# Kernel optimization log

Measured on AMD Instinct MI355X. Metric: run time of the kernel, lower is better.

Reference implementation:

```python
import jax, jax.numpy as jnp
import numpy as np

D_MODEL = 256
N_LAYERS = 4
D_STATE = 16
D_CONV = 4
EXPAND = 2
HEADDIM = 64
D_INNER = EXPAND * D_MODEL            # 512
NHEADS = D_INNER // HEADDIM           # 8
CONV_DIM = D_INNER + 2 * D_STATE      # 544 (ngroups=1)
D_IN_PROJ = 2 * D_INNER + 2 * D_STATE + NHEADS  # 1064
VOCAB = 8
MAXLEN = 2048
NCLASSES = 2
PAD_IDX = 4
EPS = 1e-5
B, L = 8, 2048


def setup_inputs() -> dict:
    key = jax.random.key(0)
    ks = jax.random.split(key, 10)
    x = jax.random.randint(ks[0], (B, L), 0, VOCAB)
    attention_mask = jnp.ones((B, L), jnp.float32)
    embedding = 0.02 * jax.random.normal(ks[1], (VOCAB, D_MODEL), jnp.float32)
    embedding = embedding.at[PAD_IDX].set(0.0)  # padding_idx row is zero
    pos_embedding = 0.02 * jax.random.normal(ks[2], (1, MAXLEN, D_MODEL), jnp.float32)
    in_proj_w = 0.05 * jax.random.normal(ks[3], (N_LAYERS, D_IN_PROJ, D_MODEL), jnp.float32)
    conv_w = 0.3 * jax.random.normal(ks[4], (N_LAYERS, CONV_DIM, D_CONV), jnp.float32)
    conv_b = jnp.zeros((N_LAYERS, CONV_DIM), jnp.float32)
    # dt_bias = softplus^{-1}(dt) with dt ~ U(0.001, 0.1), as in mamba_ssm init
    dt = jax.random.uniform(ks[5], (N_LAYERS, NHEADS), jnp.float32, 0.001, 0.1)
    dt_bias = jnp.log(jnp.expm1(dt))
    A_log = jnp.log(jax.random.uniform(ks[6], (N_LAYERS, NHEADS), jnp.float32, 1.0, 16.0))
    D_param = jnp.ones((N_LAYERS, NHEADS), jnp.float32)
    norm_w = jnp.ones((N_LAYERS, D_INNER), jnp.float32)
    out_proj_w = 0.05 * jax.random.normal(ks[7], (N_LAYERS, D_MODEL, D_INNER), jnp.float32)
    ln_w = jnp.ones((D_MODEL,), jnp.float32)
    ln_b = jnp.zeros((D_MODEL,), jnp.float32)
    cls_w = 0.05 * jax.random.normal(ks[8], (NCLASSES, D_MODEL), jnp.float32)
    cls_b = jnp.zeros((NCLASSES,), jnp.float32)
    return dict(x=x, attention_mask=attention_mask, embedding=embedding,
                pos_embedding=pos_embedding, in_proj_w=in_proj_w, conv_w=conv_w,
                conv_b=conv_b, dt_bias=dt_bias, A_log=A_log, D_param=D_param,
                norm_w=norm_w, out_proj_w=out_proj_w, ln_w=ln_w, ln_b=ln_b,
                cls_w=cls_w, cls_b=cls_b)


def _mamba2(h_in, Wi, cw, cb, dtb, Alog, Dp, nw, Wo):
    """One Mamba2 block (ngroups=1, headdim=64, norm_before_gate=False)."""
    b, l, _ = h_in.shape
    zxbcdt = jnp.einsum('bld,ed->ble', h_in, Wi)          # (b,l,1064)
    z = zxbcdt[..., :D_INNER]                             # gate
    xBC = zxbcdt[..., D_INNER:D_INNER + CONV_DIM]
    dt = jax.nn.softplus(zxbcdt[..., D_INNER + CONV_DIM:] + dtb)  # (b,l,h)
    # causal depthwise conv1d (kernel D_CONV) + silu
    xp = jnp.pad(xBC, ((0, 0), (D_CONV - 1, 0), (0, 0)))
    xwin = jnp.stack([xp[:, k:k + l, :] for k in range(D_CONV)], axis=-1)  # (b,l,c,k)
    xBC = jax.nn.silu(jnp.einsum('blck,ck->blc', xwin, cw) + cb)
    xs = xBC[..., :D_INNER].reshape(b, l, NHEADS, HEADDIM)
    Bm = xBC[..., D_INNER:D_INNER + D_STATE]              # (b,l,n)
    Cm = xBC[..., D_INNER + D_STATE:]                     # (b,l,n)
    dA = jnp.exp(dt * (-jnp.exp(Alog)))                   # (b,l,h)
    dtx = dt[..., None] * xs                              # (b,l,h,p)

    def step(h, inp):
        dA_t, dtx_t, B_t, C_t = inp
        h = dA_t[:, :, None, None] * h + dtx_t[..., None] * B_t[:, None, None, :]
        y = jnp.einsum('bhpn,bn->bhp', h, C_t)
        return h, y

    h0 = jnp.zeros((b, NHEADS, HEADDIM, D_STATE), h_in.dtype)
    _, ys = jax.lax.scan(step, h0, (jnp.swapaxes(dA, 0, 1), jnp.swapaxes(dtx, 0, 1),
                                    jnp.swapaxes(Bm, 0, 1), jnp.swapaxes(Cm, 0, 1)))
    y = jnp.swapaxes(ys, 0, 1) + Dp[None, None, :, None] * xs  # skip term D*x
    y = y.reshape(b, l, D_INNER) * jax.nn.silu(z)               # gate, then RMSNorm
    y = y * jax.lax.rsqrt(jnp.mean(jnp.square(y), axis=-1, keepdims=True) + EPS) * nw
    return jnp.einsum('ble,de->bld', y, Wo)


def _layer_norm(h, w, b):
    mu = jnp.mean(h, -1, keepdims=True)
    var = jnp.mean(jnp.square(h - mu), -1, keepdims=True)
    return (h - mu) * jax.lax.rsqrt(var + EPS) * w + b


def reference(x, attention_mask, embedding, pos_embedding, in_proj_w, conv_w,
              conv_b, dt_bias, A_log, D_param, norm_w, out_proj_w, ln_w, ln_b,
              cls_w, cls_b):
    l = x.shape[1]
    h = embedding[x] + pos_embedding[:, :l, :]
    m = attention_mask[..., None]
    h = h * m
    for i in range(N_LAYERS):
        res = h
        h = _mamba2(h, in_proj_w[i], conv_w[i], conv_b[i], dt_bias[i],
                    A_log[i], D_param[i], norm_w[i], out_proj_w[i])
        h = _layer_norm(h + res, ln_w, ln_b)
        h = h * m
    pooled = jnp.mean(h, axis=1)   # dropout is identity at eval
    return pooled @ cls_w.T + cls_b
```

## Files before the change

### kernel.cpp

```cpp
#include <hip/hip_runtime.h>
#include <hip/hip_bf16.h>
#include <math.h>

#define B_ 8
#define L_ 2048
#define DM 256
#define DIP 1064
#define DI 512
#define CD 544
#define DSZ 16
#define NH 8
#define HD 64
#define Q_ 64
#define NC 32
#define ZST 76

typedef __attribute__((ext_vector_type(8))) short bf16x8;
typedef __attribute__((ext_vector_type(4))) float f32x4;

__device__ inline unsigned short f2bf(float f) {
    __hip_bfloat16 h = __float2bfloat16(f);
    return *(unsigned short*)&h;
}
__device__ inline float bf2f(unsigned short u) {
    unsigned int x = ((unsigned int)u) << 16;
    return __uint_as_float(x);
}
__device__ inline float fast_sig(float x) {
    return __builtin_amdgcn_rcpf(1.f + __expf(-x));
}

__global__ __launch_bounds__(256) void k_f2bf(const float* __restrict__ in, unsigned short* __restrict__ out, int n4) {
    int i = blockIdx.x * 256 + threadIdx.x;
    if (i >= n4) return;
    float4 v = *(const float4*)(in + (size_t)i * 4);
    ushort4 o;
    o.x = f2bf(v.x); o.y = f2bf(v.y); o.z = f2bf(v.z); o.w = f2bf(v.w);
    *(ushort4*)(out + (size_t)i * 4) = o;
}

__global__ __launch_bounds__(256) void k_embed(const int* __restrict__ x, const float* __restrict__ mask,
                                               const float* __restrict__ emb, const float* __restrict__ pos,
                                               unsigned short* __restrict__ h_bf) {
    int i = blockIdx.x * 256 + threadIdx.x;
    if (i >= B_ * L_ * DM) return;
    int d = i % DM;
    int bl = i / DM;
    int l = bl % L_;
    int tok = x[bl];
    float v = (emb[tok * DM + d] + pos[l * DM + d]) * mask[bl];
    h_bf[i] = f2bf(v);
}

__global__ __launch_bounds__(256) void k_gemm_in(const unsigned short* __restrict__ A,
                                                 const unsigned short* __restrict__ Bw,
                                                 unsigned short* __restrict__ Cb, float* __restrict__ dtraw) {
    const int lda = DM, ldb = DM, ldc = DIP, N = DIP, K = DM;
    __shared__ __align__(16) unsigned short Lds[16384];
    unsigned short* Al = Lds;
    unsigned short* Bl = Lds + 8192;
    unsigned short* Clds = Lds;
    int tid = threadIdx.x;
    int l = tid & 63;
    int w = tid >> 6, wr = w >> 1, wc = w & 1;

    int wg = blockIdx.x;
    int xcd = wg & 7;
    int rest = wg >> 3;
    int mgrp = rest / 9;
    int n_tile = rest - mgrp * 9;
    int m_tile = xcd * 16 + mgrp;
    int m0 = m_tile * 128, n0 = n_tile * 128;

    f32x4 zero = {0.f, 0.f, 0.f, 0.f};
    f32x4 acc[4][4];
#pragma unroll
    for (int i = 0; i < 4; i++)
#pragma unroll
        for (int j = 0; j < 4; j++) acc[i][j] = zero;

    int lr = l & 15, kq = l >> 4;
    int aoff = (wr * 64 + lr) * 32 + kq * 8;
    int boff = (wc * 64 + lr) * 32 + kq * 8;

    auto stage = [&](int ks, int buf) {
        int k0 = ks * 32;
#pragma unroll
        for (int q = 0; q < 2; q++) {
            int c = tid + q * 256;
            int row = c >> 2, cc = (c & 3) * 8;
            const unsigned short* ga = A + (size_t)(m0 + row) * lda + k0 + cc;
            __builtin_amdgcn_global_load_lds((const __attribute__((address_space(1))) void*)ga,
                                             (__attribute__((address_space(3))) void*)(&Al[buf * 4096 + c * 8]), 16, 0, 0);
            int rowb = n0 + row;
            if (rowb > N - 1) rowb = N - 1;
            const unsigned short* gb = Bw + (size_t)rowb * ldb + k0 + cc;
            __builtin_amdgcn_global_load_lds((const __attribute__((address_space(1))) void*)gb,
                                             (__attribute__((address_space(3))) void*)(&Bl[buf * 4096 + c * 8]), 16, 0, 0);
        }
    };

    stage(0, 0);
    int ksteps = K / 32;
    for (int s = 0; s < ksteps; s++) {
        int buf = s & 1;
        __syncthreads();
        if (s + 1 < ksteps) stage(s + 1, buf ^ 1);
        bf16x8 a[4], b[4];
#pragma unroll
        for (int i = 0; i < 4; i++) a[i] = *(const bf16x8*)&Al[buf * 4096 + aoff + i * 512];
#pragma unroll
        for (int j = 0; j < 4; j++) b[j] = *(const bf16x8*)&Bl[buf * 4096 + boff + j * 512];
#pragma unroll
        for (int i = 0; i < 4; i++)
#pragma unroll
            for (int j = 0; j < 4; j++)
                acc[i][j] = __builtin_amdgcn_mfma_f32_16x16x32_bf16(a[i], b[j], acc[i][j], 0, 0, 0);
    }

    if (n_tile == 8) {
#pragma unroll
        for (int i = 0; i < 4; i++) {
            int m = m0 + wr * 64 + i * 16 + kq * 4;
#pragma unroll
            for (int j = 0; j < 4; j++) {
                int n = n0 + wc * 64 + j * 16 + lr;
                if (n >= DI + CD && n < N) {
#pragma unroll
                    for (int r = 0; r < 4; r++)
                        dtraw[(size_t)(m + r) * NH + (n - (DI + CD))] = acc[i][j][r];
                }
            }
        }
    }
    __syncthreads();

#pragma unroll
    for (int i = 0; i < 4; i++) {
        int row = wr * 64 + i * 16 + kq * 4;
#pragma unroll
        for (int j = 0; j < 4; j++) {
            int col = wc * 64 + j * 16 + lr;
#pragma unroll
            for (int r = 0; r < 4; r++)
                Clds[(row + r) * 128 + col] = f2bf(acc[i][j][r]);
        }
    }
    __syncthreads();

#pragma unroll
    for (int q = 0; q < 8; q++) {
        int idx = q * 256 + tid;
        int row = idx >> 4, oct = idx & 15;
        int n = n0 + oct * 8;
        if (n < N)
            *(bf16x8*)(Cb + (size_t)(m0 + row) * ldc + n) = *(const bf16x8*)&Clds[row * 128 + oct * 8];
    }
}

__global__ __launch_bounds__(256) void k_gemm_ln(const unsigned short* __restrict__ A,
                                                 const unsigned short* __restrict__ Bw,
                                                 unsigned short* __restrict__ hbf,
                                                 const float* __restrict__ lnw, const float* __restrict__ lnb,
                                                 const float* __restrict__ mask) {
    __shared__ unsigned short Al[2][32 * 32];
    __shared__ unsigned short Bl[2][256 * 32];
    __shared__ float part_s[32][4], part_q[32][4];
    int tid = threadIdx.x;
    int l = tid & 63;
    int w = tid >> 6;
    int m0 = blockIdx.x * 32;
    int lr = l & 15, kq = l >> 4;

    f32x4 zero = {0.f, 0.f, 0.f, 0.f};
    f32x4 acc[2][4];
#pragma unroll
    for (int i = 0; i < 2; i++)
#pragma unroll
        for (int j = 0; j < 4; j++) acc[i][j] = zero;

    auto stage = [&](int ks, int buf) {
        int k0 = ks * 32;
        if (tid < 128) {
            int row = tid >> 2, cc = (tid & 3) * 8;
            const unsigned short* ga = A + (size_t)(m0 + row) * DI + k0 + cc;
            __builtin_amdgcn_global_load_lds((const __attribute__((address_space(1))) void*)ga,
                                             (__attribute__((address_space(3))) void*)(&Al[buf][tid * 8]), 16, 0, 0);
        }
#pragma unroll
        for (int q = 0; q < 4; q++) {
            int c = tid + q * 256;
            int row = c >> 2, cc = (c & 3) * 8;
            const unsigned short* gb = Bw + (size_t)row * DI + k0 + cc;
            __builtin_amdgcn_global_load_lds((const __attribute__((address_space(1))) void*)gb,
                                             (__attribute__((address_space(3))) void*)(&Bl[buf][c * 8]), 16, 0, 0);
        }
    };

    stage(0, 0);
    const int ksteps = DI / 32;
    for (int s = 0; s < ksteps; s++) {
        int buf = s & 1;
        __syncthreads();
        if (s + 1 < ksteps) stage(s + 1, buf ^ 1);
        bf16x8 a[2], b[4];
#pragma unroll
        for (int i = 0; i < 2; i++) a[i] = *(const bf16x8*)&Al[buf][(i * 16 + lr) * 32 + kq * 8];
#pragma unroll
        for (int j = 0; j < 4; j++) b[j] = *(const bf16x8*)&Bl[buf][(w * 64 + j * 16 + lr) * 32 + kq * 8];
#pragma unroll
        for (int i = 0; i < 2; i++)
#pragma unroll
            for (int j = 0; j < 4; j++)
                acc[i][j] = __builtin_amdgcn_mfma_f32_16x16x32_bf16(a[i], b[j], acc[i][j], 0, 0, 0);
    }

#pragma unroll
    for (int i = 0; i < 2; i++) {
#pragma unroll
        for (int r = 0; r < 4; r++) {
            int row = i * 16 + kq * 4 + r;
            const unsigned short* hrow = hbf + (size_t)(m0 + row) * DM + w * 64 + lr;
#pragma unroll
            for (int j = 0; j < 4; j++)
                acc[i][j][r] += bf2f(hrow[j * 16]);
        }
    }
#pragma unroll
    for (int i = 0; i < 2; i++) {
#pragma unroll
        for (int r = 0; r < 4; r++) {
            float sv = acc[i][0][r] + acc[i][1][r] + acc[i][2][r] + acc[i][3][r];
            float qv = acc[i][0][r] * acc[i][0][r] + acc[i][1][r] * acc[i][1][r] +
                       acc[i][2][r] * acc[i][2][r] + acc[i][3][r] * acc[i][3][r];
#pragma unroll
            for (int off = 1; off < 16; off <<= 1) {
                sv += __shfl_xor(sv, off);
                qv += __shfl_xor(qv, off);
            }
            if (lr == 0) {
                int row = i * 16 + kq * 4 + r;
                part_s[row][w] = sv;
                part_q[row][w] = qv;
            }
        }
    }
    __syncthreads();
    float4 wv4 = make_float4(lnw[w * 64 + 0 * 16 + lr], lnw[w * 64 + 1 * 16 + lr],
                             lnw[w * 64 + 2 * 16 + lr], lnw[w * 64 + 3 * 16 + lr]);
    float4 bv4 = make_float4(lnb[w * 64 + 0 * 16 + lr], lnb[w * 64 + 1 * 16 + lr],
                             lnb[w * 64 + 2 * 16 + lr], lnb[w * 64 + 3 * 16 + lr]);
#pragma unroll
    for (int i = 0; i < 2; i++) {
#pragma unroll
        for (int r = 0; r < 4; r++) {
            int row = i * 16 + kq * 4 + r;
            float sum = part_s[row][0] + part_s[row][1] + part_s[row][2] + part_s[row][3];
            float sq  = part_q[row][0] + part_q[row][1] + part_q[row][2] + part_q[row][3];
            float mu = sum * (1.f / DM);
            float var = sq * (1.f / DM) - mu * mu;
            float rs = rsqrtf(var + 1e-5f);
            float mk = mask[m0 + row];
            unsigned short* drow = hbf + (size_t)(m0 + row) * DM + w * 64 + lr;
            float wr_[4] = {wv4.x, wv4.y, wv4.z, wv4.w};
            float br_[4] = {bv4.x, bv4.y, bv4.z, bv4.w};
#pragma unroll
            for (int j = 0; j < 4; j++) {
                float o = ((acc[i][j][r] - mu) * rs * wr_[j] + br_[j]) * mk;
                drow[j * 16] = f2bf(o);
            }
        }
    }
}

__global__ __launch_bounds__(256) void k_bcdt(const unsigned short* __restrict__ zxb,
                                              const float* __restrict__ cw, const float* __restrict__ cb,
                                              const float* __restrict__ dtraw, const float* __restrict__ dtb,
                                              const float* __restrict__ Alog,
                                              unsigned short* __restrict__ BCc,
                                              float* __restrict__ dts_g, float* __restrict__ coefS_g,
                                              float* __restrict__ cumL, float* __restrict__ Pg) {
    int pair = blockIdx.x;
    int b = pair >> 5, c = pair & 31;
    int t0 = c * Q_;
    int tid = threadIdx.x;
    int t = tid & 63, oct = tid >> 6;
    {
        int lg0 = t0 + t - 3;
        const unsigned short* base = zxb + ((size_t)b * L_ + lg0) * DIP + 1024 + oct * 8;
        bf16x8 rows[4];
#pragma unroll
        for (int k = 0; k < 4; k++) {
            if (lg0 + k >= 0) rows[k] = *(const bf16x8*)(base + (size_t)k * DIP);
            else {
#pragma unroll
                for (int j = 0; j < 8; j++) rows[k][j] = 0;
            }
        }
        bf16x8 o;
#pragma unroll
        for (int j = 0; j < 8; j++) {
            int cc = DI + oct * 8 + j;
            float acc = cb[cc];
            acc = fmaf(bf2f((unsigned short)rows[0][j]), cw[cc * 4 + 0], acc);
            acc = fmaf(bf2f((unsigned short)rows[1][j]), cw[cc * 4 + 1], acc);
            acc = fmaf(bf2f((unsigned short)rows[2][j]), cw[cc * 4 + 2], acc);
            acc = fmaf(bf2f((unsigned short)rows[3][j]), cw[cc * 4 + 3], acc);
            float s = acc * fast_sig(acc);
            o[j] = (short)f2bf(s);
        }
        *(bf16x8*)(BCc + ((size_t)(b * L_ + t0 + t)) * 32 + oct * 8) = o;
    }
#pragma unroll
    for (int ho = 0; ho < 2; ho++) {
        int h = oct * 2 + ho;
        int bh = b * 8 + h;
        float raw = dtraw[(size_t)(b * L_ + t0 + t) * NH + h] + dtb[h];
        float dtv = (raw > 20.f) ? raw : log1pf(__expf(raw));
        float v = -__expf(Alog[h]) * dtv;
#pragma unroll
        for (int off = 1; off < 64; off <<= 1) {
            float u = __shfl_up(v, off);
            if (t >= off) v += u;
        }
        float lend = __shfl(v, 63);
        size_t base = (size_t)(bh * NC + c) * Q_ + t;
        dts_g[base] = dtv;
        cumL[base] = v;
        coefS_g[base] = __expf(lend - v) * dtv;
        if (t == 63) Pg[bh * NC + c] = __expf(v);
    }
}

__global__ __launch_bounds__(256) void k_scan1c(const unsigned short* __restrict__ zxb,
                                                const unsigned short* __restrict__ BCc,
                                                const float* __restrict__ dts_g, const float* __restrict__ coefS_g,
                                                const float* __restrict__ cumL,
                                                const float* __restrict__ cw, const float* __restrict__ cb,
                                                const float* __restrict__ Dp,
                                                unsigned short* __restrict__ ybuf, unsigned short* __restrict__ Sg) {
    int wg = blockIdx.x;
    int xcd = wg & 7;
    int rest = wg >> 3;
    int slot = rest >> 3;
    int h = rest & 7;
    int pair = slot * 8 + xcd;
    int b = pair >> 5, c = pair & 31;
    int bh = b * 8 + h;
    int tid = threadIdx.x;
    int t0 = c * Q_;
    int w = tid >> 6, l = tid & 63;
    int lr = l & 15, kq = l >> 4;

    __shared__ __align__(16) unsigned short Zl[67 * ZST];
    __shared__ __align__(16) unsigned short Xt[Q_ * 72];
    __shared__ __align__(16) unsigned short Pool[4096];
    __shared__ __align__(16) unsigned short Btw[DSZ * 72];
    __shared__ float Lc[Q_], dts[Q_], coefS[Q_];
    unsigned short* Mbf = Zl;
    unsigned short* Cbf = Pool;
    unsigned short* Bbf = Pool + 2048;
    unsigned short* Ylds = Pool;

    float Dval = Dp[h];

    for (int idx = tid; idx < 67 * 8; idx += 256) {
        int rr = idx >> 3, seg = idx & 7;
        int lg = t0 - 3 + rr;
        bf16x8 v;
        if (lg >= 0) {
            v = *(const bf16x8*)(zxb + (size_t)(b * L_ + lg) * DIP + DI + h * HD + seg * 8);
        } else {
#pragma unroll
            for (int j = 0; j < 8; j++) v[j] = 0;
        }
        *(ushort4*)&Zl[rr * ZST + seg * 8]     = *(ushort4*)&v;
        *(ushort4*)&Zl[rr * ZST + seg * 8 + 4] = *((ushort4*)&v + 1);
    }
    {
        bf16x8 z8;
#pragma unroll
        for (int j = 0; j < 8; j++) z8[j] = 0;
        *(bf16x8*)&Cbf[tid * 8] = z8;
        *(bf16x8*)&Bbf[tid * 8] = z8;
    }
    if (tid < 64) {
        size_t base = (size_t)(bh * NC + c) * Q_ + tid;
        dts[tid] = dts_g[base];
        Lc[tid] = cumL[base];
        coefS[tid] = coefS_g[base];
    }
    __syncthreads();

    float xreg[4][4];
#pragma unroll
    for (int pt = 0; pt < 4; pt++) {
#pragma unroll
        for (int r = 0; r < 4; r++) {
            int t = w * 16 + kq * 4 + r;
            int p = pt * 16 + lr;
            int cc = h * HD + p;
            float acc = cb[cc];
#pragma unroll
            for (int k = 0; k < 4; k++)
                acc = fmaf(bf2f(Zl[(t + k) * ZST + p]), cw[cc * 4 + k], acc);
            float s = acc * fast_sig(acc);
            xreg[pt][r] = s;
            Xt[p * 72 + t] = f2bf(s);
        }
    }
    {
        int t = tid & 63, oct = tid >> 6;
        bf16x8 v = *(const bf16x8*)(BCc + ((size_t)(b * L_ + t0 + t)) * 32 + oct * 8);
        float dtv = dts[t], cfv = coefS[t];
#pragma unroll
        for (int j = 0; j < 8; j++) {
            int n32 = oct * 8 + j;
            float s = bf2f((unsigned short)v[j]);
            if (n32 < 16) {
                int n = n32;
                Bbf[t * 32 + (((n >> 3) ^ (t & 3)) * 8) + (n & 7)] = f2bf(dtv * s);
                Btw[n * 72 + t] = f2bf(cfv * s);
            } else {
                int n = n32 - 16;
                Cbf[t * 32 + (((n >> 3) ^ (t & 3)) * 8) + (n & 7)] = (unsigned short)v[j];
            }
        }
    }
    __syncthreads();

    f32x4 zero = {0.f, 0.f, 0.f, 0.f};

    f32x4 cbt[4];
    {
        bf16x8 af = *(const bf16x8*)&Cbf[(w * 16 + lr) * 32 + ((kq ^ (lr & 3)) * 8)];
#pragma unroll
        for (int st = 0; st < 4; st++) {
            bf16x8 bf = *(const bf16x8*)&Bbf[(st * 16 + lr) * 32 + ((kq ^ (lr & 3)) * 8)];
            cbt[st] = __builtin_amdgcn_mfma_f32_16x16x32_bf16(af, bf, zero, 0, 0, 0);
        }
    }
#pragma unroll
    for (int st = 0; st < 4; st++) {
#pragma unroll
        for (int r = 0; r < 4; r++) {
            int t = w * 16 + kq * 4 + r;
            int s = st * 16 + lr;
            float m = (s <= t) ? __expf(Lc[t] - Lc[s]) * cbt[st][r] : 0.f;
            Mbf[t * 64 + (((s >> 3) ^ (t & 7)) * 8) + (s & 7)] = f2bf(m);
        }
    }
    __syncthreads();

    {
        f32x4 acc[4];
#pragma unroll
        for (int pt = 0; pt < 4; pt++) acc[pt] = zero;
#pragma unroll
        for (int ks = 0; ks < 2; ks++) {
            bf16x8 af = *(const bf16x8*)&Mbf[(w * 16 + lr) * 64 + (((ks * 4 + kq) ^ (lr & 7)) * 8)];
#pragma unroll
            for (int pt = 0; pt < 4; pt++) {
                bf16x8 bf = *(const bf16x8*)&Xt[(pt * 16 + lr) * 72 + ks * 32 + kq * 8];
                acc[pt] = __builtin_amdgcn_mfma_f32_16x16x32_bf16(af, bf, acc[pt], 0, 0, 0);
            }
        }
#pragma unroll
        for (int pt = 0; pt < 4; pt++) {
#pragma unroll
            for (int r = 0; r < 4; r++) {
                int t = w * 16 + kq * 4 + r;
                int p = pt * 16 + lr;
                Ylds[t * 64 + p] = f2bf(acc[pt][r] + Dval * xreg[pt][r]);
            }
        }
    }

    {
        f32x4 sacc = zero;
#pragma unroll
        for (int ks = 0; ks < 2; ks++) {
            bf16x8 af = *(const bf16x8*)&Xt[(w * 16 + lr) * 72 + ks * 32 + kq * 8];
            bf16x8 bf = *(const bf16x8*)&Btw[lr * 72 + ks * 32 + kq * 8];
            sacc = __builtin_amdgcn_mfma_f32_16x16x32_bf16(af, bf, sacc, 0, 0, 0);
        }
#pragma unroll
        for (int r = 0; r < 4; r++) {
            int p = w * 16 + kq * 4 + r;
            Sg[((size_t)(bh * NC + c) * HD + p) * DSZ + lr] = f2bf(sacc[r]);
        }
    }
    __syncthreads();

    {
        unsigned short* base_y = ybuf + ((size_t)b * L_ + t0) * DI + h * HD;
#pragma unroll
        for (int q = 0; q < 2; q++) {
            int idx = q * 256 + tid;
            int t = idx >> 3, oct = idx & 7;
            *(bf16x8*)(base_y + (size_t)t * DI + oct * 8) = *(const bf16x8*)&Ylds[t * 64 + oct * 8];
        }
    }
}

__global__ __launch_bounds__(256) void k_scan2(const unsigned short* __restrict__ Sg, const float* __restrict__ Pg,
                                               unsigned short* __restrict__ Hg) {
    int bh = blockIdx.x;
    int tid = threadIdx.x;
    int p = tid >> 2, n0 = (tid & 3) * 4;
    float4 H = make_float4(0.f, 0.f, 0.f, 0.f);
    for (int g = 0; g < NC / 8; g++) {
        ushort4 S[8];
#pragma unroll
        for (int j = 0; j < 8; j++)
            S[j] = *(const ushort4*)(Sg + (((size_t)bh * NC + g * 8 + j) * HD + p) * DSZ + n0);
#pragma unroll
        for (int j = 0; j < 8; j++) {
            int cc = g * 8 + j;
            ushort4 ho;
            ho.x = f2bf(H.x); ho.y = f2bf(H.y); ho.z = f2bf(H.z); ho.w = f2bf(H.w);
            *(ushort4*)(Hg + (((size_t)bh * NC + cc) * HD + p) * DSZ + n0) = ho;
            float P = Pg[bh * NC + cc];
            H.x = fmaf(P, H.x, bf2f(S[j].x));
            H.y = fmaf(P, H.y, bf2f(S[j].y));
            H.z = fmaf(P, H.z, bf2f(S[j].z));
            H.w = fmaf(P, H.w, bf2f(S[j].w));
        }
    }
}

__global__ __launch_bounds__(256) void k_scan3g(const unsigned short* __restrict__ ybuf,
                                                const unsigned short* __restrict__ zxb,
                                                const unsigned short* __restrict__ Hg, const float* __restrict__ cumLg,
                                                const unsigned short* __restrict__ BCc, const float* __restrict__ nw,
                                                unsigned short* __restrict__ yn_bf) {
    int wg = blockIdx.x;
    int xcd = wg & 7;
    int rest = wg >> 3;
    int chunk_local = rest >> 2;
    int sub = rest & 3;
    int chunk_global = xcd * 32 + chunk_local;
    int b = chunk_global >> 5, c64 = chunk_global & 31;
    int tl0 = sub * 16;
    int t0 = c64 * 64 + sub * 16;
    int tid = threadIdx.x;
    __shared__ float Hsn[DSZ * 576];
    __shared__ float Lq[NH][16];

    {
        int p = tid & 63, hp = tid >> 6;
#pragma unroll
        for (int ho = 0; ho < 2; ho++) {
            int hh = hp * 2 + ho;
            const unsigned short* src = Hg + (((size_t)(b * NH + hh) * NC + c64) * HD + p) * DSZ;
            float* dst = &Hsn[p * 9 + hh];
            bf16x8 lo = *(const bf16x8*)(src);
            bf16x8 hi = *(const bf16x8*)(src + 8);
#pragma unroll
            for (int nq = 0; nq < 8; nq++) {
                dst[nq * 576] = bf2f((unsigned short)lo[nq]);
                dst[(nq + 8) * 576] = bf2f((unsigned short)hi[nq]);
            }
        }
    }
    if (tid < 128) {
        int hh = tid >> 4, t = tid & 15;
        Lq[hh][t] = cumLg[((size_t)(b * NH + hh) * NC + c64) * Q_ + tl0 + t];
    }
    __syncthreads();

    int t = tid >> 4, q = tid & 15;
    int hh = q >> 1, p0 = (q & 1) * 32;
    size_t bl = (size_t)b * L_ + t0 + t;
    float ef = __expf(Lq[hh][t]);

    float Cr[16];
    {
        const unsigned short* crow = BCc + bl * 32 + 16;
        bf16x8 lo = *(const bf16x8*)(crow);
        bf16x8 hi = *(const bf16x8*)(crow + 8);
#pragma unroll
        for (int k = 0; k < 8; k++) {
            Cr[k] = ef * bf2f((unsigned short)lo[k]);
            Cr[k + 8] = ef * bf2f((unsigned short)hi[k]);
        }
    }

    const unsigned short* yrow = ybuf + bl * DI + hh * HD + p0;
    const unsigned short* zrow = zxb + bl * DIP + hh * HD + p0;
    unsigned short yv[32], zv[32];
#pragma unroll
    for (int k = 0; k < 4; k++) *(bf16x8*)&yv[k * 8] = *(const bf16x8*)(yrow + k * 8);
#pragma unroll
    for (int k = 0; k < 4; k++) *(bf16x8*)&zv[k * 8] = *(const bf16x8*)(zrow + k * 8);

    float yg[32];
    float ss = 0.f;
#pragma unroll
    for (int j = 0; j < 32; j++) {
        const float* hp_ = &Hsn[(p0 + j) * 9 + hh];
        float d = 0.f;
#pragma unroll
        for (int n = 0; n < DSZ; n++) d = fmaf(Cr[n], hp_[n * 576], d);
        float y = bf2f(yv[j]) + d;
        float z = bf2f(zv[j]);
        yg[j] = y * z * fast_sig(z);
        ss = fmaf(yg[j], yg[j], ss);
    }
    ss += __shfl_xor(ss, 1);
    ss += __shfl_xor(ss, 2);
    ss += __shfl_xor(ss, 4);
    ss += __shfl_xor(ss, 8);
    float r = rsqrtf(ss * (1.f / DI) + 1e-5f);

    const float* nwp = nw + hh * HD + p0;
    unsigned short* dst = yn_bf + bl * DI + hh * HD + p0;
#pragma unroll
    for (int k = 0; k < 4; k++) {
        bf16x8 o;
#pragma unroll
        for (int j = 0; j < 8; j++) o[j] = (short)f2bf(yg[k * 8 + j] * r * nwp[k * 8 + j]);
        *(bf16x8*)(dst + k * 8) = o;
    }
}

__global__ __launch_bounds__(256) void k_pool1(const unsigned short* __restrict__ h, float* __restrict__ part) {
    int b = blockIdx.x, g = blockIdx.y, d = threadIdx.x;
    const unsigned short* hb = h + ((size_t)b * L_ + g * 128) * DM + d;
    float s = 0.f;
    for (int l = 0; l < 128; l++) s += bf2f(hb[(size_t)l * DM]);
    part[((size_t)b * 16 + g) * DM + d] = s;
}

__global__ __launch_bounds__(256) void k_pool2(const float* __restrict__ part, const float* __restrict__ cw,
                                               const float* __restrict__ cb, float* __restrict__ out) {
    int b = blockIdx.x, tid = threadIdx.x;
    float s = 0.f;
#pragma unroll
    for (int g = 0; g < 16; g++) s += part[((size_t)b * 16 + g) * DM + tid];
    s *= (1.0f / L_);
    float p0 = s * cw[tid];
    float p1 = s * cw[DM + tid];
#pragma unroll
    for (int m = 1; m < 64; m <<= 1) {
        p0 += __shfl_xor(p0, m);
        p1 += __shfl_xor(p1, m);
    }
    __shared__ float r0[4], r1[4];
    if ((tid & 63) == 0) { r0[tid >> 6] = p0; r1[tid >> 6] = p1; }
    __syncthreads();
    if (tid == 0) {
        out[b * 2 + 0] = r0[0] + r0[1] + r0[2] + r0[3] + cb[0];
        out[b * 2 + 1] = r1[0] + r1[1] + r1[2] + r1[3] + cb[1];
    }
}

extern "C" void kernel_launch(void* const* d_in, const int* in_sizes, int n_in,
                              void* d_out, int out_size, void* d_ws, size_t ws_size,
                              hipStream_t stream) {
    const int*   x    = (const int*)d_in[0];
    const float* mask = (const float*)d_in[1];
    const float* emb  = (const float*)d_in[2];
    const float* pos  = (const float*)d_in[3];
    const float* Wi   = (const float*)d_in[4];
    const float* cw   = (const float*)d_in[5];
    const float* cb   = (const float*)d_in[6];
    const float* dtb  = (const float*)d_in[7];
    const float* Alog = (const float*)d_in[8];
    const float* Dp   = (const float*)d_in[9];
    const float* nw   = (const float*)d_in[10];
    const float* Wo   = (const float*)d_in[11];
    const float* lnw  = (const float*)d_in[12];
    const float* lnb  = (const float*)d_in[13];
    const float* clsw = (const float*)d_in[14];
    const float* clsb = (const float*)d_in[15];
    float* out = (float*)d_out;

    float* ws     = (float*)d_ws;
    float* dtraw  = ws;
    float* Pg     = dtraw + (size_t)B_ * L_ * NH;
    float* cumL   = Pg + (size_t)64 * NC;
    float* dts_g  = cumL + (size_t)64 * NC * Q_;
    float* coefSg = dts_g + (size_t)64 * NC * Q_;
    float* pool   = coefSg + (size_t)64 * NC * Q_;
    unsigned short* Sg    = (unsigned short*)(pool + (size_t)B_ * 16 * DM);
    unsigned short* Hg    = Sg + (size_t)64 * NC * HD * DSZ;
    unsigned short* BCc   = Hg + (size_t)64 * NC * HD * DSZ;
    unsigned short* zxb   = BCc + (size_t)B_ * L_ * 32;
    unsigned short* ybuf  = zxb + (size_t)B_ * L_ * DIP;
    unsigned short* h_bf  = ybuf + (size_t)B_ * L_ * DI;
    unsigned short* yn_bf = h_bf + (size_t)B_ * L_ * DM;
    unsigned short* Wi_bf = yn_bf + (size_t)B_ * L_ * DI;
    unsigned short* Wo_bf = Wi_bf + (size_t)4 * DIP * DM;

    k_f2bf<<<(4 * DIP * DM / 4 + 255) / 256, 256, 0, stream>>>(Wi, Wi_bf, 4 * DIP * DM / 4);
    k_f2bf<<<(4 * DM * DI / 4 + 255) / 256, 256, 0, stream>>>(Wo, Wo_bf, 4 * DM * DI / 4);

    k_embed<<<(B_ * L_ * DM + 255) / 256, 256, 0, stream>>>(x, mask, emb, pos, h_bf);

    for (int i = 0; i < 4; i++) {
        k_gemm_in<<<128 * 9, 256, 0, stream>>>(
            h_bf, Wi_bf + (size_t)i * DIP * DM, zxb, dtraw);
        k_bcdt<<<B_ * NC, 256, 0, stream>>>(
            zxb, cw + (size_t)i * CD * 4, cb + i * CD, dtraw, dtb + i * NH, Alog + i * NH,
            BCc, dts_g, coefSg, cumL, Pg);
        k_scan1c<<<2048, 256, 0, stream>>>(
            zxb, BCc, dts_g, coefSg, cumL, cw + (size_t)i * CD * 4, cb + i * CD,
            Dp + i * NH, ybuf, Sg);
        k_scan2<<<64, 256, 0, stream>>>(Sg, Pg, Hg);
        k_scan3g<<<1024, 256, 0, stream>>>(ybuf, zxb, Hg, cumL, BCc, nw + (size_t)i * DI, yn_bf);
        k_gemm_ln<<<B_ * L_ / 32, 256, 0, stream>>>(
            yn_bf, Wo_bf + (size_t)i * DM * DI, h_bf, lnw, lnb, mask);
    }

    k_pool1<<<dim3(B_, 16), 256, 0, stream>>>(h_bf, pool);
    k_pool2<<<B_, 256, 0, stream>>>(pool, clsw, clsb, out);
}
```

Before: 350.9 us.

## Fuse scan output gating/RMSNorm with out-projection GEMM and LayerNorm

Merges the final scan stage (state contribution, gating, RMSNorm) with the out-projection GEMM plus residual LayerNorm into one kernel. Each block now handles 32 timesteps, keeps the normalized y tile in LDS as the GEMM A operand, and reuses the Hsn shared buffer for double-buffered weight staging. This removes the yn_bf global round trip and one launch per layer. In exchange, LDS use per block grows, the grid halves to 512 blocks, and each block reloads the full out-projection weight.

```diff
diff --git a/kernel.cpp b/kernel.cpp
--- a/kernel.cpp
+++ b/kernel.cpp
@@ -14,6 +14,7 @@
 #define Q_ 64
 #define NC 32
 #define ZST 76
+#define YST 528
 
 typedef __attribute__((ext_vector_type(8))) short bf16x8;
 typedef __attribute__((ext_vector_type(4))) float f32x4;
@@ -155,121 +156,6 @@
         int n = n0 + oct * 8;
         if (n < N)
             *(bf16x8*)(Cb + (size_t)(m0 + row) * ldc + n) = *(const bf16x8*)&Clds[row * 128 + oct * 8];
-    }
-}
-
-__global__ __launch_bounds__(256) void k_gemm_ln(const unsigned short* __restrict__ A,
-                                                 const unsigned short* __restrict__ Bw,
-                                                 unsigned short* __restrict__ hbf,
-                                                 const float* __restrict__ lnw, const float* __restrict__ lnb,
-                                                 const float* __restrict__ mask) {
-    __shared__ unsigned short Al[2][32 * 32];
-    __shared__ unsigned short Bl[2][256 * 32];
-    __shared__ float part_s[32][4], part_q[32][4];
-    int tid = threadIdx.x;
-    int l = tid & 63;
-    int w = tid >> 6;
-    int m0 = blockIdx.x * 32;
-    int lr = l & 15, kq = l >> 4;
-
-    f32x4 zero = {0.f, 0.f, 0.f, 0.f};
-    f32x4 acc[2][4];
-#pragma unroll
-    for (int i = 0; i < 2; i++)
-#pragma unroll
-        for (int j = 0; j < 4; j++) acc[i][j] = zero;
-
-    auto stage = [&](int ks, int buf) {
-        int k0 = ks * 32;
-        if (tid < 128) {
-            int row = tid >> 2, cc = (tid & 3) * 8;
-            const unsigned short* ga = A + (size_t)(m0 + row) * DI + k0 + cc;
-            __builtin_amdgcn_global_load_lds((const __attribute__((address_space(1))) void*)ga,
-                                             (__attribute__((address_space(3))) void*)(&Al[buf][tid * 8]), 16, 0, 0);
-        }
-#pragma unroll
-        for (int q = 0; q < 4; q++) {
-            int c = tid + q * 256;
-            int row = c >> 2, cc = (c & 3) * 8;
-            const unsigned short* gb = Bw + (size_t)row * DI + k0 + cc;
-            __builtin_amdgcn_global_load_lds((const __attribute__((address_space(1))) void*)gb,
-                                             (__attribute__((address_space(3))) void*)(&Bl[buf][c * 8]), 16, 0, 0);
-        }
-    };
-
-    stage(0, 0);
-    const int ksteps = DI / 32;
-    for (int s = 0; s < ksteps; s++) {
-        int buf = s & 1;
-        __syncthreads();
-        if (s + 1 < ksteps) stage(s + 1, buf ^ 1);
-        bf16x8 a[2], b[4];
-#pragma unroll
-        for (int i = 0; i < 2; i++) a[i] = *(const bf16x8*)&Al[buf][(i * 16 + lr) * 32 + kq * 8];
-#pragma unroll
-        for (int j = 0; j < 4; j++) b[j] = *(const bf16x8*)&Bl[buf][(w * 64 + j * 16 + lr) * 32 + kq * 8];
-#pragma unroll
-        for (int i = 0; i < 2; i++)
-#pragma unroll
-            for (int j = 0; j < 4; j++)
-                acc[i][j] = __builtin_amdgcn_mfma_f32_16x16x32_bf16(a[i], b[j], acc[i][j], 0, 0, 0);
-    }
-
-#pragma unroll
-    for (int i = 0; i < 2; i++) {
-#pragma unroll
-        for (int r = 0; r < 4; r++) {
-            int row = i * 16 + kq * 4 + r;
-            const unsigned short* hrow = hbf + (size_t)(m0 + row) * DM + w * 64 + lr;
-#pragma unroll
-            for (int j = 0; j < 4; j++)
-                acc[i][j][r] += bf2f(hrow[j * 16]);
-        }
-    }
-#pragma unroll
-    for (int i = 0; i < 2; i++) {
-#pragma unroll
-        for (int r = 0; r < 4; r++) {
-            float sv = acc[i][0][r] + acc[i][1][r] + acc[i][2][r] + acc[i][3][r];
-            float qv = acc[i][0][r] * acc[i][0][r] + acc[i][1][r] * acc[i][1][r] +
-                       acc[i][2][r] * acc[i][2][r] + acc[i][3][r] * acc[i][3][r];
-#pragma unroll
-            for (int off = 1; off < 16; off <<= 1) {
-                sv += __shfl_xor(sv, off);
-                qv += __shfl_xor(qv, off);
-            }
-            if (lr == 0) {
-                int row = i * 16 + kq * 4 + r;
-                part_s[row][w] = sv;
-                part_q[row][w] = qv;
-            }
-        }
-    }
-    __syncthreads();
-    float4 wv4 = make_float4(lnw[w * 64 + 0 * 16 + lr], lnw[w * 64 + 1 * 16 + lr],
-                             lnw[w * 64 + 2 * 16 + lr], lnw[w * 64 + 3 * 16 + lr]);
-    float4 bv4 = make_float4(lnb[w * 64 + 0 * 16 + lr], lnb[w * 64 + 1 * 16 + lr],
-                             lnb[w * 64 + 2 * 16 + lr], lnb[w * 64 + 3 * 16 + lr]);
-#pragma unroll
-    for (int i = 0; i < 2; i++) {
-#pragma unroll
-        for (int r = 0; r < 4; r++) {
-            int row = i * 16 + kq * 4 + r;
-            float sum = part_s[row][0] + part_s[row][1] + part_s[row][2] + part_s[row][3];
-            float sq  = part_q[row][0] + part_q[row][1] + part_q[row][2] + part_q[row][3];
-            float mu = sum * (1.f / DM);
-            float var = sq * (1.f / DM) - mu * mu;
-            float rs = rsqrtf(var + 1e-5f);
-            float mk = mask[m0 + row];
-            unsigned short* drow = hbf + (size_t)(m0 + row) * DM + w * 64 + lr;
-            float wr_[4] = {wv4.x, wv4.y, wv4.z, wv4.w};
-            float br_[4] = {bv4.x, bv4.y, bv4.z, bv4.w};
-#pragma unroll
-            for (int j = 0; j < 4; j++) {
-                float o = ((acc[i][j][r] - mu) * rs * wr_[j] + br_[j]) * mk;
-                drow[j * 16] = f2bf(o);
-            }
-        }
     }
 }
 
@@ -529,23 +415,30 @@
     }
 }
 
-__global__ __launch_bounds__(256) void k_scan3g(const unsigned short* __restrict__ ybuf,
-                                                const unsigned short* __restrict__ zxb,
-                                                const unsigned short* __restrict__ Hg, const float* __restrict__ cumLg,
-                                                const unsigned short* __restrict__ BCc, const float* __restrict__ nw,
-                                                unsigned short* __restrict__ yn_bf) {
+__global__ __launch_bounds__(256) void k_scan3gl(const unsigned short* __restrict__ ybuf,
+                                                 const unsigned short* __restrict__ zxb,
+                                                 const unsigned short* __restrict__ Hg,
+                                                 const float* __restrict__ cumLg,
+                                                 const unsigned short* __restrict__ BCc,
+                                                 const float* __restrict__ nw,
+                                                 const unsigned short* __restrict__ Wo,
+                                                 unsigned short* __restrict__ hbf,
+                                                 const float* __restrict__ lnw, const float* __restrict__ lnb,
+                                                 const float* __restrict__ mask) {
     int wg = blockIdx.x;
     int xcd = wg & 7;
     int rest = wg >> 3;
-    int chunk_local = rest >> 2;
-    int sub = rest & 3;
-    int chunk_global = xcd * 32 + chunk_local;
+    int chunk_global = xcd * 32 + (rest >> 1);
+    int sub = rest & 1;
     int b = chunk_global >> 5, c64 = chunk_global & 31;
-    int tl0 = sub * 16;
-    int t0 = c64 * 64 + sub * 16;
+    int t0 = c64 * 64 + sub * 32;
     int tid = threadIdx.x;
-    __shared__ float Hsn[DSZ * 576];
-    __shared__ float Lq[NH][16];
+
+    __shared__ __align__(16) float Hsn[DSZ * 576];
+    __shared__ __align__(16) unsigned short Ylds[32 * YST];
+    __shared__ float Lq[NH][32];
+    __shared__ float part_s[32][4], part_q[32][4];
+    unsigned short* Bl = (unsigned short*)Hsn;
 
     {
         int p = tid & 63, hp = tid >> 6;
@@ -563,64 +456,168 @@
             }
         }
     }
-    if (tid < 128) {
-        int hh = tid >> 4, t = tid & 15;
-        Lq[hh][t] = cumLg[((size_t)(b * NH + hh) * NC + c64) * Q_ + tl0 + t];
-    }
-    __syncthreads();
-
-    int t = tid >> 4, q = tid & 15;
-    int hh = q >> 1, p0 = (q & 1) * 32;
-    size_t bl = (size_t)b * L_ + t0 + t;
-    float ef = __expf(Lq[hh][t]);
-
-    float Cr[16];
-    {
-        const unsigned short* crow = BCc + bl * 32 + 16;
-        bf16x8 lo = *(const bf16x8*)(crow);
-        bf16x8 hi = *(const bf16x8*)(crow + 8);
-#pragma unroll
-        for (int k = 0; k < 8; k++) {
-            Cr[k] = ef * bf2f((unsigned short)lo[k]);
-            Cr[k + 8] = ef * bf2f((unsigned short)hi[k]);
-        }
-    }
-
-    const unsigned short* yrow = ybuf + bl * DI + hh * HD + p0;
-    const unsigned short* zrow = zxb + bl * DIP + hh * HD + p0;
-    unsigned short yv[32], zv[32];
-#pragma unroll
-    for (int k = 0; k < 4; k++) *(bf16x8*)&yv[k * 8] = *(const bf16x8*)(yrow + k * 8);
-#pragma unroll
-    for (int k = 0; k < 4; k++) *(bf16x8*)&zv[k * 8] = *(const bf16x8*)(zrow + k * 8);
-
-    float yg[32];
-    float ss = 0.f;
-#pragma unroll
-    for (int j = 0; j < 32; j++) {
-        const float* hp_ = &Hsn[(p0 + j) * 9 + hh];
-        float d = 0.f;
-#pragma unroll
-        for (int n = 0; n < DSZ; n++) d = fmaf(Cr[n], hp_[n * 576], d);
-        float y = bf2f(yv[j]) + d;
-        float z = bf2f(zv[j]);
-        yg[j] = y * z * fast_sig(z);
-        ss = fmaf(yg[j], yg[j], ss);
-    }
-    ss += __shfl_xor(ss, 1);
-    ss += __shfl_xor(ss, 2);
-    ss += __shfl_xor(ss, 4);
-    ss += __shfl_xor(ss, 8);
-    float r = rsqrtf(ss * (1.f / DI) + 1e-5f);
-
-    const float* nwp = nw + hh * HD + p0;
-    unsigned short* dst = yn_bf + bl * DI + hh * HD + p0;
-#pragma unroll
-    for (int k = 0; k < 4; k++) {
-        bf16x8 o;
-#pragma unroll
-        for (int j = 0; j < 8; j++) o[j] = (short)f2bf(yg[k * 8 + j] * r * nwp[k * 8 + j]);
-        *(bf16x8*)(dst + k * 8) = o;
+    {
+        int hh = tid >> 5, t = tid & 31;
+        Lq[hh][t] = cumLg[((size_t)(b * NH + hh) * NC + c64) * Q_ + sub * 32 + t];
+    }
+    __syncthreads();
+
+    int trow = tid >> 4, q16 = tid & 15;
+    int hh = q16 >> 1, p0 = (q16 & 1) * 32;
+
+#pragma unroll
+    for (int rg = 0; rg < 2; rg++) {
+        int tl = rg * 16 + trow;
+        size_t bl = (size_t)b * L_ + t0 + tl;
+        float ef = __expf(Lq[hh][tl]);
+
+        float Cr[16];
+        {
+            const unsigned short* crow = BCc + bl * 32 + 16;
+            bf16x8 lo = *(const bf16x8*)(crow);
+            bf16x8 hi = *(const bf16x8*)(crow + 8);
+#pragma unroll
+            for (int k = 0; k < 8; k++) {
+                Cr[k] = ef * bf2f((unsigned short)lo[k]);
+                Cr[k + 8] = ef * bf2f((unsigned short)hi[k]);
+            }
+        }
+
+        const unsigned short* yrow = ybuf + bl * DI + hh * HD + p0;
+        const unsigned short* zrow = zxb + bl * DIP + hh * HD + p0;
+        unsigned short yv[32], zv[32];
+#pragma unroll
+        for (int k = 0; k < 4; k++) *(bf16x8*)&yv[k * 8] = *(const bf16x8*)(yrow + k * 8);
+#pragma unroll
+        for (int k = 0; k < 4; k++) *(bf16x8*)&zv[k * 8] = *(const bf16x8*)(zrow + k * 8);
+
+        float yg[32];
+        float ss = 0.f;
+#pragma unroll
+        for (int j = 0; j < 32; j++) {
+            const float* hp_ = &Hsn[(p0 + j) * 9 + hh];
+            float d = 0.f;
+#pragma unroll
+            for (int n = 0; n < DSZ; n++) d = fmaf(Cr[n], hp_[n * 576], d);
+            float y = bf2f(yv[j]) + d;
+            float z = bf2f(zv[j]);
+            yg[j] = y * z * fast_sig(z);
+            ss = fmaf(yg[j], yg[j], ss);
+        }
+        ss += __shfl_xor(ss, 1);
+        ss += __shfl_xor(ss, 2);
+        ss += __shfl_xor(ss, 4);
+        ss += __shfl_xor(ss, 8);
+        float r = rsqrtf(ss * (1.f / DI) + 1e-5f);
+
+        const float* nwp = nw + hh * HD + p0;
+#pragma unroll
+        for (int k = 0; k < 4; k++) {
+            bf16x8 o;
+#pragma unroll
+            for (int j = 0; j < 8; j++) o[j] = (short)f2bf(yg[k * 8 + j] * r * nwp[k * 8 + j]);
+            *(bf16x8*)&Ylds[tl * YST + hh * HD + p0 + k * 8] = o;
+        }
+    }
+    __syncthreads();
+
+    int l = tid & 63;
+    int w = tid >> 6;
+    int lr = l & 15, kq = l >> 4;
+    int m0row = b * L_ + t0;
+
+    f32x4 zero = {0.f, 0.f, 0.f, 0.f};
+    f32x4 acc[2][4];
+#pragma unroll
+    for (int i = 0; i < 2; i++)
+#pragma unroll
+        for (int j = 0; j < 4; j++) acc[i][j] = zero;
+
+    auto stage = [&](int ks, int buf) {
+        int k0 = ks * 32;
+#pragma unroll
+        for (int q = 0; q < 4; q++) {
+            int c = tid + q * 256;
+            int row = c >> 2, cc = (c & 3) * 8;
+            const unsigned short* gb = Wo + (size_t)row * DI + k0 + cc;
+            __builtin_amdgcn_global_load_lds((const __attribute__((address_space(1))) void*)gb,
+                                             (__attribute__((address_space(3))) void*)(&Bl[buf * 8192 + c * 8]), 16, 0, 0);
+        }
+    };
+
+    stage(0, 0);
+    const int ksteps = DI / 32;
+    for (int s = 0; s < ksteps; s++) {
+        int buf = s & 1;
+        __syncthreads();
+        if (s + 1 < ksteps) stage(s + 1, buf ^ 1);
+        bf16x8 a[2], bfr[4];
+#pragma unroll
+        for (int i = 0; i < 2; i++) a[i] = *(const bf16x8*)&Ylds[(i * 16 + lr) * YST + s * 32 + kq * 8];
+#pragma unroll
+        for (int j = 0; j < 4; j++) bfr[j] = *(const bf16x8*)&Bl[buf * 8192 + (w * 64 + j * 16 + lr) * 32 + kq * 8];
+#pragma unroll
+        for (int i = 0; i < 2; i++)
+#pragma unroll
+            for (int j = 0; j < 4; j++)
+                acc[i][j] = __builtin_amdgcn_mfma_f32_16x16x32_bf16(a[i], bfr[j], acc[i][j], 0, 0, 0);
+    }
+
+#pragma unroll
+    for (int i = 0; i < 2; i++) {
+#pragma unroll
+        for (int r = 0; r < 4; r++) {
+            int row = i * 16 + kq * 4 + r;
+            const unsigned short* hrow = hbf + (size_t)(m0row + row) * DM + w * 64 + lr;
+#pragma unroll
+            for (int j = 0; j < 4; j++)
+                acc[i][j][r] += bf2f(hrow[j * 16]);
+        }
+    }
+#pragma unroll
+    for (int i = 0; i < 2; i++) {
+#pragma unroll
+        for (int r = 0; r < 4; r++) {
+            float sv = acc[i][0][r] + acc[i][1][r] + acc[i][2][r] + acc[i][3][r];
+            float qv = acc[i][0][r] * acc[i][0][r] + acc[i][1][r] * acc[i][1][r] +
+                       acc[i][2][r] * acc[i][2][r] + acc[i][3][r] * acc[i][3][r];
+#pragma unroll
+            for (int off = 1; off < 16; off <<= 1) {
+                sv += __shfl_xor(sv, off);
+                qv += __shfl_xor(qv, off);
+            }
+            if (lr == 0) {
+                int row = i * 16 + kq * 4 + r;
+                part_s[row][w] = sv;
+                part_q[row][w] = qv;
+            }
+        }
+    }
+    __syncthreads();
+    float4 wv4 = make_float4(lnw[w * 64 + 0 * 16 + lr], lnw[w * 64 + 1 * 16 + lr],
+                             lnw[w * 64 + 2 * 16 + lr], lnw[w * 64 + 3 * 16 + lr]);
+    float4 bv4 = make_float4(lnb[w * 64 + 0 * 16 + lr], lnb[w * 64 + 1 * 16 + lr],
+                             lnb[w * 64 + 2 * 16 + lr], lnb[w * 64 + 3 * 16 + lr]);
+#pragma unroll
+    for (int i = 0; i < 2; i++) {
+#pragma unroll
+        for (int r = 0; r < 4; r++) {
+            int row = i * 16 + kq * 4 + r;
+            float sum = part_s[row][0] + part_s[row][1] + part_s[row][2] + part_s[row][3];
+            float sq  = part_q[row][0] + part_q[row][1] + part_q[row][2] + part_q[row][3];
+            float mu = sum * (1.f / DM);
+            float var = sq * (1.f / DM) - mu * mu;
+            float rs = rsqrtf(var + 1e-5f);
+            float mk = mask[m0row + row];
+            unsigned short* drow = hbf + (size_t)(m0row + row) * DM + w * 64 + lr;
+            float wr_[4] = {wv4.x, wv4.y, wv4.z, wv4.w};
+            float br_[4] = {bv4.x, bv4.y, bv4.z, bv4.w};
+#pragma unroll
+            for (int j = 0; j < 4; j++) {
+                float o = ((acc[i][j][r] - mu) * rs * wr_[j] + br_[j]) * mk;
+                drow[j * 16] = f2bf(o);
+            }
+        }
     }
 }
 
@@ -689,8 +686,7 @@
     unsigned short* zxb   = BCc + (size_t)B_ * L_ * 32;
     unsigned short* ybuf  = zxb + (size_t)B_ * L_ * DIP;
     unsigned short* h_bf  = ybuf + (size_t)B_ * L_ * DI;
-    unsigned short* yn_bf = h_bf + (size_t)B_ * L_ * DM;
-    unsigned short* Wi_bf = yn_bf + (size_t)B_ * L_ * DI;
+    unsigned short* Wi_bf = h_bf + (size_t)B_ * L_ * DM;
     unsigned short* Wo_bf = Wi_bf + (size_t)4 * DIP * DM;
 
     k_f2bf<<<(4 * DIP * DM / 4 + 255) / 256, 256, 0, stream>>>(Wi, Wi_bf, 4 * DIP * DM / 4);
@@ -708,9 +704,9 @@
             zxb, BCc, dts_g, coefSg, cumL, cw + (size_t)i * CD * 4, cb + i * CD,
             Dp + i * NH, ybuf, Sg);
         k_scan2<<<64, 256, 0, stream>>>(Sg, Pg, Hg);
-        k_scan3g<<<1024, 256, 0, stream>>>(ybuf, zxb, Hg, cumL, BCc, nw + (size_t)i * DI, yn_bf);
-        k_gemm_ln<<<B_ * L_ / 32, 256, 0, stream>>>(
-            yn_bf, Wo_bf + (size_t)i * DM * DI, h_bf, lnw, lnb, mask);
+        k_scan3gl<<<512, 256, 0, stream>>>(
+            ybuf, zxb, Hg, cumL, BCc, nw + (size_t)i * DI,
+            Wo_bf + (size_t)i * DM * DI, h_bf, lnw, lnb, mask);
     }
 
     k_pool1<<<dim3(B_, 16), 256, 0, stream>>>(h_bf, pool);
```

After: 1.062 ms. +202.7%, slower.
